# Kernel optimization log

Measured on AMD Instinct MI355X. Metric: run time of the kernel, lower is better.

Reference implementation:

```python
import jax, jax.numpy as jnp
import numpy as np

N_NODES = 100000

def _gcn_norm(edge_index, num_nodes):
    # add self-loops, compute symmetric normalization coeffs per edge
    loops = jnp.arange(num_nodes, dtype=edge_index.dtype)
    src = jnp.concatenate([edge_index[0], loops])
    dst = jnp.concatenate([edge_index[1], loops])
    deg = jax.ops.segment_sum(jnp.ones_like(dst, dtype=jnp.float32), dst,
                              num_segments=num_nodes)
    dinv = jnp.where(deg > 0, jax.lax.rsqrt(deg), 0.0)
    norm = dinv[src] * dinv[dst]  # [E + N]
    return src, dst, norm

def _gcn_conv(x, W, b, src, dst, norm, num_nodes):
    h = x @ W                              # [N, out] transform first (PyG order)
    msg = h[src] * norm[:, None]           # gather + scale
    out = jax.ops.segment_sum(msg, dst, num_segments=num_nodes)  # scatter-add
    return out + b

def setup_inputs() -> dict:
    key = jax.random.key(0)
    k1, k2, k3, k4 = jax.random.split(key, 4)
    F_in, H, C = 128, 64, 40
    x = jax.random.normal(k1, (N_NODES, F_in), dtype=jnp.float32)
    edge_index = jax.random.randint(k2, (2, 1600000), 0, N_NODES, dtype=jnp.int64)
    W1 = jax.random.normal(k3, (F_in, H), dtype=jnp.float32) / np.sqrt(F_in)
    b1 = jnp.zeros((H,), dtype=jnp.float32)
    W2 = jax.random.normal(k4, (H, C), dtype=jnp.float32) / np.sqrt(H)
    b2 = jnp.zeros((C,), dtype=jnp.float32)
    return {"x": x, "edge_index": edge_index, "W1": W1, "b1": b1, "W2": W2, "b2": b2}

def reference(x, edge_index, W1, b1, W2, b2):
    num_nodes = x.shape[0]
    src, dst, norm = _gcn_norm(edge_index, num_nodes)
    h = _gcn_conv(x, W1, b1, src, dst, norm, num_nodes)
    h = jax.nn.relu(h)
    # dropout is identity in eval mode (training=False)
    h = _gcn_conv(h, W2, b2, src, dst, norm, num_nodes)
    return jax.nn.log_softmax(h, axis=1)
```

## Files before the change

### kernel.cpp

```cpp
#include <hip/hip_runtime.h>
#include <math.h>

#define NPB 256
#define BSH 8
#define MAXNB 400
#define BIN_CHUNK 8192
#define HIST_CHUNK 16384

typedef __attribute__((ext_vector_type(8))) short bf16x8;
typedef __attribute__((ext_vector_type(4))) float f32x4;
typedef __attribute__((ext_vector_type(2))) float f32x2;

__device__ __forceinline__ unsigned short f2bf(float f){
  unsigned int u = __float_as_uint(f);
  unsigned int r = (u + 0x7FFFu + ((u >> 16) & 1u)) >> 16;
  return (unsigned short)r;
}

__device__ __forceinline__ bf16x8 cvt8(float4 a, float4 b){
  union { unsigned u[4]; bf16x8 v; } r;
  asm("v_cvt_pk_bf16_f32 %0, %1, %2" : "=v"(r.u[0]) : "v"(a.x), "v"(a.y));
  asm("v_cvt_pk_bf16_f32 %0, %1, %2" : "=v"(r.u[1]) : "v"(a.z), "v"(a.w));
  asm("v_cvt_pk_bf16_f32 %0, %1, %2" : "=v"(r.u[2]) : "v"(b.x), "v"(b.y));
  asm("v_cvt_pk_bf16_f32 %0, %1, %2" : "=v"(r.u[3]) : "v"(b.z), "v"(b.w));
  return r.v;
}

__global__ void k_prep(const float* __restrict__ W1, const float* __restrict__ W2,
                       unsigned short* __restrict__ w1t, unsigned short* __restrict__ w2t,
                       int* __restrict__ bcnt, int NB){
  int t = threadIdx.x;
  if(blockIdx.x == 0){
    for(int i = t; i < 8192; i += 256){
      int k = i >> 6, f = i & 63;
      w1t[f*128 + k] = f2bf(W1[i]);
    }
  } else {
    for(int i = t; i < 3072; i += 256){
      int c = i >> 6, k = i & 63;
      w2t[c*64 + k] = (c < 40) ? f2bf(W2[k*40 + c]) : (unsigned short)0;
    }
    for(int i = t; i < NB; i += 256) bcnt[i] = 0;
  }
}


__global__ __launch_bounds__(256) void k_bhist(const int* __restrict__ dst, int E,
                                               int* __restrict__ bcnt, int NB){
  __shared__ int l[MAXNB];
  int t = threadIdx.x;
  int base = blockIdx.x*HIST_CHUNK;
  int end = base + HIST_CHUNK; if(end > E) end = E;
  for(int b = t; b < NB; b += 256) l[b] = 0;
  __syncthreads();
  for(int i = base + t; i < end; i += 256) atomicAdd(&l[dst[i] >> BSH], 1);
  __syncthreads();
  for(int b = t; b < NB; b += 256){ int c = l[b]; if(c) atomicAdd(&bcnt[b], c); }
}

__global__ void k_bscan(const int* __restrict__ bcnt, int* __restrict__ bofs,
                        int* __restrict__ bcur, int NB, int E){
  __shared__ int sh[1024];
  int t = threadIdx.x;
  int c0 = (2*t   < NB) ? bcnt[2*t]   : 0;
  int c1 = (2*t+1 < NB) ? bcnt[2*t+1] : 0;
  sh[t] = c0 + c1; __syncthreads();
  for(int off = 1; off < 1024; off <<= 1){
    int v = (t >= off) ? sh[t - off] : 0;
    __syncthreads();
    sh[t] += v;
    __syncthreads();
  }
  int pairEx = sh[t] - (c0 + c1);
  if(2*t   < NB){ bofs[2*t]   = pairEx;      bcur[2*t]   = pairEx; }
  if(2*t+1 < NB){ bofs[2*t+1] = pairEx + c0; bcur[2*t+1] = pairEx + c0; }
  if(t == 0) bofs[NB] = E;
}

__global__ __launch_bounds__(256) void k_binpass(const int* __restrict__ src,
                          const int* __restrict__ dst, int E,
                          int* __restrict__ bcur, unsigned int* __restrict__ binned, int NB){
  __shared__ int lcnt[MAXNB];
  __shared__ int lpos[MAXNB];
  int t = threadIdx.x;
  int base = blockIdx.x * BIN_CHUNK;
  int end = base + BIN_CHUNK; if(end > E) end = E;
  for(int b = t; b < NB; b += 256) lcnt[b] = 0;
  __syncthreads();
  for(int i = base + t; i < end; i += 256)
    atomicAdd(&lcnt[dst[i] >> BSH], 1);
  __syncthreads();
  for(int b = t; b < NB; b += 256){
    int c = lcnt[b];
    lpos[b] = c ? atomicAdd(&bcur[b], c) : 0;
  }
  __syncthreads();
  for(int i = base + t; i < end; i += 256){
    int d = dst[i];
    int b = d >> BSH;
    unsigned int rec = (unsigned int)src[i] | ((unsigned int)(d & (NPB-1)) << 17);
    int p = atomicAdd(&lpos[b], 1);
    binned[p] = rec;
  }
}

__global__ __launch_bounds__(256) void k_bscatter(const unsigned int* __restrict__ binned,
     const int* __restrict__ bofs, int* __restrict__ csr, int* __restrict__ row_ofs,
     float* __restrict__ dinv, int N, int E, int NB){
  __shared__ int lcnt[NPB];
  __shared__ int lofs[NPB];
  __shared__ int lcur[NPB];
  __shared__ int wsum[4];
  int b = blockIdx.x, t = threadIdx.x;
  int beg = bofs[b], end = bofs[b+1];
  lcnt[t] = 0;
  __syncthreads();
  for(int i = beg + t; i < end; i += 256) atomicAdd(&lcnt[binned[i] >> 17], 1);
  __syncthreads();
  int c = lcnt[t];
  int lane = t & 63, wid = t >> 6;
  int v = c;
  #pragma unroll
  for(int off = 1; off < 64; off <<= 1){
    int nv = __shfl_up(v, off, 64);
    if(lane >= off) v += nv;
  }
  if(lane == 63) wsum[wid] = v;
  __syncthreads();
  int wpre = 0;
  #pragma unroll
  for(int k2 = 0; k2 < 4; k2++) if(k2 < wid) wpre += wsum[k2];
  int ex = wpre + v - c;
  lofs[t] = beg + ex; lcur[t] = 0;
  int node = (b << BSH) + t;
  if(node < N){
    row_ofs[node] = beg + ex;
    dinv[node] = rsqrtf((float)(c + 1));
  }
  __syncthreads();
  for(int i = beg + t; i < end; i += 256){
    unsigned int rec = binned[i];
    int dl = rec >> 17;
    int pos = lofs[dl] + atomicAdd(&lcur[dl], 1);
    csr[pos] = (int)(rec & 0x1FFFFu);
  }
  if(b == NB-1 && t == 0) row_ofs[N] = E;
}

__global__ __launch_bounds__(256) void k_gemm1(const float* __restrict__ x,
                        const unsigned short* __restrict__ w1t,
                        const float* __restrict__ dinv, unsigned int* __restrict__ g1, int n){
  __shared__ unsigned short xs[128*136];
  __shared__ unsigned short wt[64*136];
  int tid = threadIdx.x;
  int nodeBase = blockIdx.x*128;
  for(int i = tid; i < 1024; i += 256){
    int f = i >> 4, seg = i & 15;
    *(uint4*)&wt[f*136 + seg*8] = *(const uint4*)&w1t[f*128 + seg*8];
  }
  {
    const float4* x4 = (const float4*)x;
    for(int i = tid; i < 2048; i += 256){
      int node = i >> 4, seg = i & 15;
      float4 va = make_float4(0.f,0.f,0.f,0.f), vb = va;
      if(nodeBase + node < n){
        va = x4[(size_t)(nodeBase + node)*32 + seg*2];
        vb = x4[(size_t)(nodeBase + node)*32 + seg*2 + 1];
      }
      *(bf16x8*)&xs[node*136 + seg*8] = cvt8(va, vb);
    }
  }
  __syncthreads();

  int w = tid >> 6, lane = tid & 63;
  int ml = lane & 15, q = lane >> 4;
  int n0 = nodeBase + w*32 + ml;
  int n1 = n0 + 16;
  bool vn0 = n0 < n, vn1 = n1 < n;

  f32x4 a00 = {0.f,0.f,0.f,0.f}, a01 = {0.f,0.f,0.f,0.f},
        a02 = {0.f,0.f,0.f,0.f}, a03 = {0.f,0.f,0.f,0.f};
  f32x4 a10 = {0.f,0.f,0.f,0.f}, a11 = {0.f,0.f,0.f,0.f},
        a12 = {0.f,0.f,0.f,0.f}, a13 = {0.f,0.f,0.f,0.f};
  const unsigned short* brow = &xs[(w*32 + ml)*136 + q*8];
  const unsigned short* arow = &wt[ml*136 + q*8];
  #pragma unroll
  for(int s = 0; s < 4; s++){
    bf16x8 bb0 = *(const bf16x8*)(brow +        s*32);
    bf16x8 bb1 = *(const bf16x8*)(brow + 2176 + s*32);
    bf16x8 a0 = *(const bf16x8*)(arow +    0 + s*32);
    bf16x8 a1 = *(const bf16x8*)(arow + 2176 + s*32);
    bf16x8 a2 = *(const bf16x8*)(arow + 4352 + s*32);
    bf16x8 a3 = *(const bf16x8*)(arow + 6528 + s*32);
    a00 = __builtin_amdgcn_mfma_f32_16x16x32_bf16(a0, bb0, a00, 0, 0, 0);
    a01 = __builtin_amdgcn_mfma_f32_16x16x32_bf16(a1, bb0, a01, 0, 0, 0);
    a02 = __builtin_amdgcn_mfma_f32_16x16x32_bf16(a2, bb0, a02, 0, 0, 0);
    a03 = __builtin_amdgcn_mfma_f32_16x16x32_bf16(a3, bb0, a03, 0, 0, 0);
    a10 = __builtin_amdgcn_mfma_f32_16x16x32_bf16(a0, bb1, a10, 0, 0, 0);
    a11 = __builtin_amdgcn_mfma_f32_16x16x32_bf16(a1, bb1, a11, 0, 0, 0);
    a12 = __builtin_amdgcn_mfma_f32_16x16x32_bf16(a2, bb1, a12, 0, 0, 0);
    a13 = __builtin_amdgcn_mfma_f32_16x16x32_bf16(a3, bb1, a13, 0, 0, 0);
  }
  if(vn0){
    float dv = dinv[n0];
    unsigned base16 = ((unsigned)n0 << 4) + q;
    int p;
    p = __builtin_amdgcn_cvt_pk_fp8_f32(a00[0]*dv, a00[1]*dv, 0, false);
    p = __builtin_amdgcn_cvt_pk_fp8_f32(a00[2]*dv, a00[3]*dv, p, true);
    g1[base16 +  0] = (unsigned)p;
    p = __builtin_amdgcn_cvt_pk_fp8_f32(a01[0]*dv, a01[1]*dv, 0, false);
    p = __builtin_amdgcn_cvt_pk_fp8_f32(a01[2]*dv, a01[3]*dv, p, true);
    g1[base16 +  4] = (unsigned)p;
    p = __builtin_amdgcn_cvt_pk_fp8_f32(a02[0]*dv, a02[1]*dv, 0, false);
    p = __builtin_amdgcn_cvt_pk_fp8_f32(a02[2]*dv, a02[3]*dv, p, true);
    g1[base16 +  8] = (unsigned)p;
    p = __builtin_amdgcn_cvt_pk_fp8_f32(a03[0]*dv, a03[1]*dv, 0, false);
    p = __builtin_amdgcn_cvt_pk_fp8_f32(a03[2]*dv, a03[3]*dv, p, true);
    g1[base16 + 12] = (unsigned)p;
  }
  if(vn1){
    float dv = dinv[n1];
    unsigned base16 = ((unsigned)n1 << 4) + q;
    int p;
    p = __builtin_amdgcn_cvt_pk_fp8_f32(a10[0]*dv, a10[1]*dv, 0, false);
    p = __builtin_amdgcn_cvt_pk_fp8_f32(a10[2]*dv, a10[3]*dv, p, true);
    g1[base16 +  0] = (unsigned)p;
    p = __builtin_amdgcn_cvt_pk_fp8_f32(a11[0]*dv, a11[1]*dv, 0, false);
    p = __builtin_amdgcn_cvt_pk_fp8_f32(a11[2]*dv, a11[3]*dv, p, true);
    g1[base16 +  4] = (unsigned)p;
    p = __builtin_amdgcn_cvt_pk_fp8_f32(a12[0]*dv, a12[1]*dv, 0, false);
    p = __builtin_amdgcn_cvt_pk_fp8_f32(a12[2]*dv, a12[3]*dv, p, true);
    g1[base16 +  8] = (unsigned)p;
    p = __builtin_amdgcn_cvt_pk_fp8_f32(a13[0]*dv, a13[1]*dv, 0, false);
    p = __builtin_amdgcn_cvt_pk_fp8_f32(a13[2]*dv, a13[3]*dv, p, true);
    g1[base16 + 12] = (unsigned)p;
  }
}

__global__ __launch_bounds__(256) void k_agg1g2(const unsigned* __restrict__ g1,
    const int* __restrict__ row_ofs, const int* __restrict__ csr,
    const float* __restrict__ dinv, const float* __restrict__ b1,
    const unsigned short* __restrict__ w2t, unsigned char* __restrict__ g2, int n){
  __shared__ unsigned short us[64*72];
  __shared__ unsigned short ws2[48*72];
  int t = threadIdx.x;
  int nodeBase = blockIdx.x*64;
  for(int i = t; i < 384; i += 256){
    int row = i >> 3, seg = i & 7;
    *(uint4*)&ws2[row*72 + seg*8] = *(const uint4*)&w2t[row*64 + seg*8];
  }
  int lane = t & 63;
  int f = lane & 15;
  int bq = (lane & 48) << 2;
  int qg = t >> 4;
  float4 bb1 = ((const float4*)b1)[f];
  #pragma unroll 1
  for(int i = 0; i < 4; i++){
    int node = nodeBase + qg*4 + i;
    int lrow = qg*4 + i;
    if(node < n){
      int beg = row_ofs[node], end = row_ofs[node+1];
      unsigned v = g1[((unsigned)node << 4) + f];
      f32x2 s01 = __builtin_amdgcn_cvt_pk_f32_fp8(v, false);
      f32x2 s23 = __builtin_amdgcn_cvt_pk_f32_fp8(v, true);
      for(int e = beg; e < end; e += 16){
        int rem = end - e; if(rem > 16) rem = 16;
        int idxv = (f < rem) ? csr[e + f] : 0;
        int j = 0;
        for(; j + 4 <= rem; j += 4){
          int r0 = __builtin_amdgcn_ds_bpermute(bq + ((j+0) << 2), idxv);
          int r1 = __builtin_amdgcn_ds_bpermute(bq + ((j+1) << 2), idxv);
          int r2 = __builtin_amdgcn_ds_bpermute(bq + ((j+2) << 2), idxv);
          int r3 = __builtin_amdgcn_ds_bpermute(bq + ((j+3) << 2), idxv);
          unsigned v0 = g1[((unsigned)r0 << 4) + f];
          unsigned v1 = g1[((unsigned)r1 << 4) + f];
          unsigned v2 = g1[((unsigned)r2 << 4) + f];
          unsigned v3 = g1[((unsigned)r3 << 4) + f];
          s01 += __builtin_amdgcn_cvt_pk_f32_fp8(v0, false);
          s23 += __builtin_amdgcn_cvt_pk_f32_fp8(v0, true);
          s01 += __builtin_amdgcn_cvt_pk_f32_fp8(v1, false);
          s23 += __builtin_amdgcn_cvt_pk_f32_fp8(v1, true);
          s01 += __builtin_amdgcn_cvt_pk_f32_fp8(v2, false);
          s23 += __builtin_amdgcn_cvt_pk_f32_fp8(v2, true);
          s01 += __builtin_amdgcn_cvt_pk_f32_fp8(v3, false);
          s23 += __builtin_amdgcn_cvt_pk_f32_fp8(v3, true);
        }
        for(; j < rem; j++){
          int r0 = __builtin_amdgcn_ds_bpermute(bq + (j << 2), idxv);
          unsigned v0 = g1[((unsigned)r0 << 4) + f];
          s01 += __builtin_amdgcn_cvt_pk_f32_fp8(v0, false);
          s23 += __builtin_amdgcn_cvt_pk_f32_fp8(v0, true);
        }
      }
      float dv = dinv[node];
      float h0 = fmaxf(fmaf(dv, s01.x, bb1.x), 0.f);
      float h1 = fmaxf(fmaf(dv, s01.y, bb1.y), 0.f);
      float h2 = fmaxf(fmaf(dv, s23.x, bb1.z), 0.f);
      float h3 = fmaxf(fmaf(dv, s23.y, bb1.w), 0.f);
      unsigned p0, p1;
      asm("v_cvt_pk_bf16_f32 %0, %1, %2" : "=v"(p0) : "v"(dv*h0), "v"(dv*h1));
      asm("v_cvt_pk_bf16_f32 %0, %1, %2" : "=v"(p1) : "v"(dv*h2), "v"(dv*h3));
      *(uint2*)&us[lrow*72 + f*4] = make_uint2(p0, p1);
    } else {
      *(uint2*)&us[lrow*72 + f*4] = make_uint2(0u, 0u);
    }
  }
  __syncthreads();
  int w = t >> 6;
  int ml = lane & 15, q = lane >> 4;
  f32x4 acc0 = {0.f,0.f,0.f,0.f}, acc1 = {0.f,0.f,0.f,0.f}, acc2 = {0.f,0.f,0.f,0.f};
  const unsigned short* brow = &us[(w*16 + ml)*72 + q*8];
  const unsigned short* a0r = &ws2[ml*72 + q*8];
  #pragma unroll
  for(int s = 0; s < 2; s++){
    bf16x8 bb = *(const bf16x8*)(brow + s*32);
    bf16x8 a0 = *(const bf16x8*)(a0r +    0 + s*32);
    bf16x8 a1 = *(const bf16x8*)(a0r + 1152 + s*32);
    bf16x8 a2 = *(const bf16x8*)(a0r + 2304 + s*32);
    acc0 = __builtin_amdgcn_mfma_f32_16x16x32_bf16(a0, bb, acc0, 0, 0, 0);
    acc1 = __builtin_amdgcn_mfma_f32_16x16x32_bf16(a1, bb, acc1, 0, 0, 0);
    acc2 = __builtin_amdgcn_mfma_f32_16x16x32_bf16(a2, bb, acc2, 0, 0, 0);
  }
  int node = nodeBase + w*16 + ml;
  if(node < n){
    unsigned* gd = (unsigned*)g2;
    unsigned rb = (unsigned)node*10u + q;
    int p;
    p = __builtin_amdgcn_cvt_pk_fp8_f32(acc0[0], acc0[1], 0, false);
    p = __builtin_amdgcn_cvt_pk_fp8_f32(acc0[2], acc0[3], p, true);
    gd[rb + 0] = (unsigned)p;
    p = __builtin_amdgcn_cvt_pk_fp8_f32(acc1[0], acc1[1], 0, false);
    p = __builtin_amdgcn_cvt_pk_fp8_f32(acc1[2], acc1[3], p, true);
    gd[rb + 4] = (unsigned)p;
    if(q < 2){
      p = __builtin_amdgcn_cvt_pk_fp8_f32(acc2[0], acc2[1], 0, false);
      p = __builtin_amdgcn_cvt_pk_fp8_f32(acc2[2], acc2[3], p, true);
      gd[rb + 8] = (unsigned)p;
    }
  }
}

__global__ __launch_bounds__(256) void k_agg2(const unsigned char* __restrict__ g2,
     const int* __restrict__ row_ofs, const int* __restrict__ csr,
     const float* __restrict__ dinv, const float* __restrict__ b2,
     float* __restrict__ out, int N){
  int t = threadIdx.x;
  int lane = t & 63;
  int f = lane & 15;
  int fc = (f < 10) ? f : 0;
  int bq = (lane & 48) << 2;
  int node = blockIdx.x*16 + (t >> 4);
  if(node >= N) return;
  int beg = row_ofs[node], end = row_ofs[node+1];
  const unsigned* gd = (const unsigned*)g2;
  unsigned v = gd[(unsigned)node*10u + fc];
  f32x2 s01 = __builtin_amdgcn_cvt_pk_f32_fp8(v, false);
  f32x2 s23 = __builtin_amdgcn_cvt_pk_f32_fp8(v, true);
  for(int e = beg; e < end; e += 16){
    int rem = end - e; if(rem > 16) rem = 16;
    int idxv = (f < rem) ? csr[e + f] : 0;
    int j = 0;
    for(; j + 4 <= rem; j += 4){
      int r0 = __builtin_amdgcn_ds_bpermute(bq + ((j+0) << 2), idxv);
      int r1 = __builtin_amdgcn_ds_bpermute(bq + ((j+1) << 2), idxv);
      int r2 = __builtin_amdgcn_ds_bpermute(bq + ((j+2) << 2), idxv);
      int r3 = __builtin_amdgcn_ds_bpermute(bq + ((j+3) << 2), idxv);
      unsigned v0 = gd[(unsigned)r0*10u + fc];
      unsigned v1 = gd[(unsigned)r1*10u + fc];
      unsigned v2 = gd[(unsigned)r2*10u + fc];
      unsigned v3 = gd[(unsigned)r3*10u + fc];
      s01 += __builtin_amdgcn_cvt_pk_f32_fp8(v0, false);
      s23 += __builtin_amdgcn_cvt_pk_f32_fp8(v0, true);
      s01 += __builtin_amdgcn_cvt_pk_f32_fp8(v1, false);
      s23 += __builtin_amdgcn_cvt_pk_f32_fp8(v1, true);
      s01 += __builtin_amdgcn_cvt_pk_f32_fp8(v2, false);
      s23 += __builtin_amdgcn_cvt_pk_f32_fp8(v2, true);
      s01 += __builtin_amdgcn_cvt_pk_f32_fp8(v3, false);
      s23 += __builtin_amdgcn_cvt_pk_f32_fp8(v3, true);
    }
    for(; j < rem; j++){
      int r0 = __builtin_amdgcn_ds_bpermute(bq + (j << 2), idxv);
      unsigned v0 = gd[(unsigned)r0*10u + fc];
      s01 += __builtin_amdgcn_cvt_pk_f32_fp8(v0, false);
      s23 += __builtin_amdgcn_cvt_pk_f32_fp8(v0, true);
    }
  }
  float dv = dinv[node];
  float4 bb = ((const float4*)b2)[fc];
  float l0 = fmaf(dv, s01.x, bb.x);
  float l1 = fmaf(dv, s01.y, bb.y);
  float l2 = fmaf(dv, s23.x, bb.z);
  float l3 = fmaf(dv, s23.y, bb.w);
  bool valid = (f < 10);
  float m = valid ? fmaxf(fmaxf(l0,l1), fmaxf(l2,l3)) : -INFINITY;
  m = fmaxf(m, __shfl_xor(m,1,64)); m = fmaxf(m, __shfl_xor(m,2,64));
  m = fmaxf(m, __shfl_xor(m,4,64)); m = fmaxf(m, __shfl_xor(m,8,64));
  float ex = valid ? (expf(l0-m)+expf(l1-m)) + (expf(l2-m)+expf(l3-m)) : 0.f;
  ex += __shfl_xor(ex,1,64); ex += __shfl_xor(ex,2,64);
  ex += __shfl_xor(ex,4,64); ex += __shfl_xor(ex,8,64);
  float ll = logf(ex);
  if(valid){
    ((float4*)out)[(unsigned)node*10u + f] = make_float4(l0-m-ll, l1-m-ll, l2-m-ll, l3-m-ll);
  }
}


extern "C" void kernel_launch(void* const* d_in, const int* in_sizes, int n_in,
                              void* d_out, int out_size, void* d_ws, size_t ws_size,
                              hipStream_t stream){
  const float* x  = (const float*)d_in[0];
  const int*   ei = (const int*)  d_in[1];
  const float* W1 = (const float*)d_in[2];
  const float* b1 = (const float*)d_in[3];
  const float* W2 = (const float*)d_in[4];
  const float* b2 = (const float*)d_in[5];
  float* out = (float*)d_out;

  int N = in_sizes[0] / 128;
  int E = in_sizes[1] / 2;
  const int* src = ei;
  const int* dst = ei + E;
  int NB = (N + NPB - 1) >> BSH;

  char* w = (char*)d_ws;
  auto alloc = [&](size_t bytes) -> char* {
    char* p = w;
    w += (bytes + 511) & ~(size_t)511;
    return p;
  };
  int*   bcnt    = (int*)  alloc((size_t)NB*4);
  int*   bofs    = (int*)  alloc((size_t)(NB+1)*4);
  int*   bcur    = (int*)  alloc((size_t)NB*4);
  int*   row_ofs = (int*)  alloc((size_t)(N+1)*4);
  float* dinv    = (float*)alloc((size_t)N*4);
  unsigned int* binned = (unsigned int*)alloc((size_t)E*4);
  int*   csr     = (int*)  alloc((size_t)E*4);
  unsigned int*   g1 = (unsigned int*)  alloc((size_t)N*64);
  unsigned char*  g2 = (unsigned char*) alloc((size_t)N*40);
  unsigned short* w1t = (unsigned short*)alloc((size_t)64*128*2);
  unsigned short* w2t = (unsigned short*)alloc((size_t)48*64*2);

  k_prep    <<<2, 256, 0, stream>>>(W1, W2, w1t, w2t, bcnt, NB);
  k_bhist   <<<(E+HIST_CHUNK-1)/HIST_CHUNK, 256, 0, stream>>>(dst, E, bcnt, NB);
  k_bscan   <<<1, 1024, 0, stream>>>(bcnt, bofs, bcur, NB, E);
  k_binpass <<<(E+BIN_CHUNK-1)/BIN_CHUNK, 256, 0, stream>>>(src, dst, E, bcur, binned, NB);
  k_bscatter<<<NB, 256, 0, stream>>>(binned, bofs, csr, row_ofs, dinv, N, E, NB);

  k_gemm1   <<<(N+127)/128, 256, 0, stream>>>(x, w1t, dinv, g1, N);
  k_agg1g2  <<<(N+63)/64, 256, 0, stream>>>(g1, row_ofs, csr, dinv, b1, w2t, g2, N);
  k_agg2    <<<(N+15)/16, 256, 0, stream>>>(g2, row_ofs, csr, dinv, b2, out, N);
}
```

Before: 228.1 us.

## Add dynamic per-block node work queues to aggregation kernels and fold prep into histogram

Both aggregation kernels now hand out nodes dynamically. Each 16-lane quarter-wave claims the next node from a shared atomic counter and processes one 16-edge chunk per iteration, so uneven node degrees balance within the block. agg2 now covers 64 nodes per block instead of 16. The weight prep kernel is merged into the histogram launch as extra blocks, and bcnt zeroing moves to a memset. Histogram and bin chunk sizes are halved or quartered to create more blocks. The change adds an atomic, a shuffle and wave-wide vote overhead to every loop iteration.

```diff
diff --git a/kernel.cpp b/kernel.cpp
--- a/kernel.cpp
+++ b/kernel.cpp
@@ -4,8 +4,8 @@
 #define NPB 256
 #define BSH 8
 #define MAXNB 400
-#define BIN_CHUNK 8192
-#define HIST_CHUNK 16384
+#define BIN_CHUNK 4096
+#define HIST_CHUNK 4096
 
 typedef __attribute__((ext_vector_type(8))) short bf16x8;
 typedef __attribute__((ext_vector_type(4))) float f32x4;
@@ -26,36 +26,36 @@
   return r.v;
 }
 
-__global__ void k_prep(const float* __restrict__ W1, const float* __restrict__ W2,
-                       unsigned short* __restrict__ w1t, unsigned short* __restrict__ w2t,
-                       int* __restrict__ bcnt, int NB){
-  int t = threadIdx.x;
-  if(blockIdx.x == 0){
-    for(int i = t; i < 8192; i += 256){
-      int k = i >> 6, f = i & 63;
-      w1t[f*128 + k] = f2bf(W1[i]);
-    }
-  } else {
-    for(int i = t; i < 3072; i += 256){
-      int c = i >> 6, k = i & 63;
-      w2t[c*64 + k] = (c < 40) ? f2bf(W2[k*40 + c]) : (unsigned short)0;
-    }
-    for(int i = t; i < NB; i += 256) bcnt[i] = 0;
-  }
-}
-
 
 __global__ __launch_bounds__(256) void k_bhist(const int* __restrict__ dst, int E,
-                                               int* __restrict__ bcnt, int NB){
+                                               int* __restrict__ bcnt, int NB, int NBH,
+                                               const float* __restrict__ W1,
+                                               const float* __restrict__ W2,
+                                               unsigned short* __restrict__ w1t,
+                                               unsigned short* __restrict__ w2t){
   __shared__ int l[MAXNB];
-  int t = threadIdx.x;
-  int base = blockIdx.x*HIST_CHUNK;
+  int t = threadIdx.x, b = blockIdx.x;
+  if(b >= NBH){
+    if(b == NBH){
+      for(int i = t; i < 8192; i += 256){
+        int k = i >> 6, f = i & 63;
+        w1t[f*128 + k] = f2bf(W1[i]);
+      }
+    } else {
+      for(int i = t; i < 3072; i += 256){
+        int c = i >> 6, k = i & 63;
+        w2t[c*64 + k] = (c < 40) ? f2bf(W2[k*40 + c]) : (unsigned short)0;
+      }
+    }
+    return;
+  }
+  int base = b*HIST_CHUNK;
   int end = base + HIST_CHUNK; if(end > E) end = E;
-  for(int b = t; b < NB; b += 256) l[b] = 0;
+  for(int i = t; i < NB; i += 256) l[i] = 0;
   __syncthreads();
   for(int i = base + t; i < end; i += 256) atomicAdd(&l[dst[i] >> BSH], 1);
   __syncthreads();
-  for(int b = t; b < NB; b += 256){ int c = l[b]; if(c) atomicAdd(&bcnt[b], c); }
+  for(int i = t; i < NB; i += 256){ int c = l[i]; if(c) atomicAdd(&bcnt[i], c); }
 }
 
 __global__ void k_bscan(const int* __restrict__ bcnt, int* __restrict__ bofs,
@@ -243,39 +243,60 @@
     const unsigned short* __restrict__ w2t, unsigned char* __restrict__ g2, int n){
   __shared__ unsigned short us[64*72];
   __shared__ unsigned short ws2[48*72];
+  __shared__ int nctr;
   int t = threadIdx.x;
   int nodeBase = blockIdx.x*64;
   for(int i = t; i < 384; i += 256){
     int row = i >> 3, seg = i & 7;
     *(uint4*)&ws2[row*72 + seg*8] = *(const uint4*)&w2t[row*64 + seg*8];
   }
+  if(t == 0) nctr = 0;
+  __syncthreads();
   int lane = t & 63;
-  int f = lane & 15;
-  int bq = (lane & 48) << 2;
-  int qg = t >> 4;
-  float4 bb1 = ((const float4*)b1)[f];
-  #pragma unroll 1
-  for(int i = 0; i < 4; i++){
-    int node = nodeBase + qg*4 + i;
-    int lrow = qg*4 + i;
-    if(node < n){
-      int beg = row_ofs[node], end = row_ofs[node+1];
-      unsigned v = g1[((unsigned)node << 4) + f];
-      f32x2 s01 = __builtin_amdgcn_cvt_pk_f32_fp8(v, false);
-      f32x2 s23 = __builtin_amdgcn_cvt_pk_f32_fp8(v, true);
-      for(int e = beg; e < end; e += 16){
-        int rem = end - e; if(rem > 16) rem = 16;
-        int idxv = (f < rem) ? csr[e + f] : 0;
+  int lq = lane & 15;
+  int qsrc = lane & 48;
+  int bq = qsrc << 2;
+  float4 bb1 = ((const float4*)b1)[lq];
+  int myi = -1;
+  int e = 0, eend = 0;
+  float dv = 0.f;
+  f32x2 s01 = {0.f,0.f}, s23 = {0.f,0.f};
+  for(;;){
+    if(myi == -1){
+      int tk = 0;
+      if(lq == 0) tk = atomicAdd(&nctr, 1);
+      tk = __shfl(tk, qsrc, 64);
+      if(tk >= 64){ myi = -2; }
+      else {
+        myi = tk;
+        int node = nodeBase + tk;
+        if(node < n){
+          e = row_ofs[node]; eend = row_ofs[node+1];
+          dv = dinv[node];
+          unsigned v = g1[((unsigned)node << 4) + lq];
+          s01 = __builtin_amdgcn_cvt_pk_f32_fp8(v, false);
+          s23 = __builtin_amdgcn_cvt_pk_f32_fp8(v, true);
+        } else {
+          e = 0; eend = 0; dv = 0.f;
+          s01 = (f32x2){0.f,0.f}; s23 = (f32x2){0.f,0.f};
+        }
+      }
+    }
+    if(__all(myi == -2)) break;
+    if(myi >= 0){
+      int rem = eend - e; if(rem > 16) rem = 16;
+      if(rem > 0){
+        int idxv = (lq < rem) ? csr[e + lq] : 0;
         int j = 0;
         for(; j + 4 <= rem; j += 4){
           int r0 = __builtin_amdgcn_ds_bpermute(bq + ((j+0) << 2), idxv);
           int r1 = __builtin_amdgcn_ds_bpermute(bq + ((j+1) << 2), idxv);
           int r2 = __builtin_amdgcn_ds_bpermute(bq + ((j+2) << 2), idxv);
           int r3 = __builtin_amdgcn_ds_bpermute(bq + ((j+3) << 2), idxv);
-          unsigned v0 = g1[((unsigned)r0 << 4) + f];
-          unsigned v1 = g1[((unsigned)r1 << 4) + f];
-          unsigned v2 = g1[((unsigned)r2 << 4) + f];
-          unsigned v3 = g1[((unsigned)r3 << 4) + f];
+          unsigned v0 = g1[((unsigned)r0 << 4) + lq];
+          unsigned v1 = g1[((unsigned)r1 << 4) + lq];
+          unsigned v2 = g1[((unsigned)r2 << 4) + lq];
+          unsigned v3 = g1[((unsigned)r3 << 4) + lq];
           s01 += __builtin_amdgcn_cvt_pk_f32_fp8(v0, false);
           s23 += __builtin_amdgcn_cvt_pk_f32_fp8(v0, true);
           s01 += __builtin_amdgcn_cvt_pk_f32_fp8(v1, false);
@@ -287,22 +308,23 @@
         }
         for(; j < rem; j++){
           int r0 = __builtin_amdgcn_ds_bpermute(bq + (j << 2), idxv);
-          unsigned v0 = g1[((unsigned)r0 << 4) + f];
+          unsigned v0 = g1[((unsigned)r0 << 4) + lq];
           s01 += __builtin_amdgcn_cvt_pk_f32_fp8(v0, false);
           s23 += __builtin_amdgcn_cvt_pk_f32_fp8(v0, true);
         }
-      }
-      float dv = dinv[node];
-      float h0 = fmaxf(fmaf(dv, s01.x, bb1.x), 0.f);
-      float h1 = fmaxf(fmaf(dv, s01.y, bb1.y), 0.f);
-      float h2 = fmaxf(fmaf(dv, s23.x, bb1.z), 0.f);
-      float h3 = fmaxf(fmaf(dv, s23.y, bb1.w), 0.f);
-      unsigned p0, p1;
-      asm("v_cvt_pk_bf16_f32 %0, %1, %2" : "=v"(p0) : "v"(dv*h0), "v"(dv*h1));
-      asm("v_cvt_pk_bf16_f32 %0, %1, %2" : "=v"(p1) : "v"(dv*h2), "v"(dv*h3));
-      *(uint2*)&us[lrow*72 + f*4] = make_uint2(p0, p1);
-    } else {
-      *(uint2*)&us[lrow*72 + f*4] = make_uint2(0u, 0u);
+        e += rem;
+      }
+      if(e >= eend){
+        float h0 = fmaxf(fmaf(dv, s01.x, bb1.x), 0.f);
+        float h1 = fmaxf(fmaf(dv, s01.y, bb1.y), 0.f);
+        float h2 = fmaxf(fmaf(dv, s23.x, bb1.z), 0.f);
+        float h3 = fmaxf(fmaf(dv, s23.y, bb1.w), 0.f);
+        unsigned p0, p1;
+        asm("v_cvt_pk_bf16_f32 %0, %1, %2" : "=v"(p0) : "v"(dv*h0), "v"(dv*h1));
+        asm("v_cvt_pk_bf16_f32 %0, %1, %2" : "=v"(p1) : "v"(dv*h2), "v"(dv*h3));
+        *(uint2*)&us[myi*72 + lq*4] = make_uint2(p0, p1);
+        myi = -1;
+      }
     }
   }
   __syncthreads();
@@ -344,63 +366,97 @@
      const int* __restrict__ row_ofs, const int* __restrict__ csr,
      const float* __restrict__ dinv, const float* __restrict__ b2,
      float* __restrict__ out, int N){
+  __shared__ int nctr;
   int t = threadIdx.x;
+  if(t == 0) nctr = 0;
+  __syncthreads();
   int lane = t & 63;
-  int f = lane & 15;
-  int fc = (f < 10) ? f : 0;
-  int bq = (lane & 48) << 2;
-  int node = blockIdx.x*16 + (t >> 4);
-  if(node >= N) return;
-  int beg = row_ofs[node], end = row_ofs[node+1];
+  int lq = lane & 15;
+  int fc = (lq < 10) ? lq : 0;
+  int qsrc = lane & 48;
+  int bq = qsrc << 2;
+  int nodeBase = blockIdx.x*64;
   const unsigned* gd = (const unsigned*)g2;
-  unsigned v = gd[(unsigned)node*10u + fc];
-  f32x2 s01 = __builtin_amdgcn_cvt_pk_f32_fp8(v, false);
-  f32x2 s23 = __builtin_amdgcn_cvt_pk_f32_fp8(v, true);
-  for(int e = beg; e < end; e += 16){
-    int rem = end - e; if(rem > 16) rem = 16;
-    int idxv = (f < rem) ? csr[e + f] : 0;
-    int j = 0;
-    for(; j + 4 <= rem; j += 4){
-      int r0 = __builtin_amdgcn_ds_bpermute(bq + ((j+0) << 2), idxv);
-      int r1 = __builtin_amdgcn_ds_bpermute(bq + ((j+1) << 2), idxv);
-      int r2 = __builtin_amdgcn_ds_bpermute(bq + ((j+2) << 2), idxv);
-      int r3 = __builtin_amdgcn_ds_bpermute(bq + ((j+3) << 2), idxv);
-      unsigned v0 = gd[(unsigned)r0*10u + fc];
-      unsigned v1 = gd[(unsigned)r1*10u + fc];
-      unsigned v2 = gd[(unsigned)r2*10u + fc];
-      unsigned v3 = gd[(unsigned)r3*10u + fc];
-      s01 += __builtin_amdgcn_cvt_pk_f32_fp8(v0, false);
-      s23 += __builtin_amdgcn_cvt_pk_f32_fp8(v0, true);
-      s01 += __builtin_amdgcn_cvt_pk_f32_fp8(v1, false);
-      s23 += __builtin_amdgcn_cvt_pk_f32_fp8(v1, true);
-      s01 += __builtin_amdgcn_cvt_pk_f32_fp8(v2, false);
-      s23 += __builtin_amdgcn_cvt_pk_f32_fp8(v2, true);
-      s01 += __builtin_amdgcn_cvt_pk_f32_fp8(v3, false);
-      s23 += __builtin_amdgcn_cvt_pk_f32_fp8(v3, true);
-    }
-    for(; j < rem; j++){
-      int r0 = __builtin_amdgcn_ds_bpermute(bq + (j << 2), idxv);
-      unsigned v0 = gd[(unsigned)r0*10u + fc];
-      s01 += __builtin_amdgcn_cvt_pk_f32_fp8(v0, false);
-      s23 += __builtin_amdgcn_cvt_pk_f32_fp8(v0, true);
-    }
-  }
-  float dv = dinv[node];
-  float4 bb = ((const float4*)b2)[fc];
-  float l0 = fmaf(dv, s01.x, bb.x);
-  float l1 = fmaf(dv, s01.y, bb.y);
-  float l2 = fmaf(dv, s23.x, bb.z);
-  float l3 = fmaf(dv, s23.y, bb.w);
-  bool valid = (f < 10);
-  float m = valid ? fmaxf(fmaxf(l0,l1), fmaxf(l2,l3)) : -INFINITY;
-  m = fmaxf(m, __shfl_xor(m,1,64)); m = fmaxf(m, __shfl_xor(m,2,64));
-  m = fmaxf(m, __shfl_xor(m,4,64)); m = fmaxf(m, __shfl_xor(m,8,64));
-  float ex = valid ? (expf(l0-m)+expf(l1-m)) + (expf(l2-m)+expf(l3-m)) : 0.f;
-  ex += __shfl_xor(ex,1,64); ex += __shfl_xor(ex,2,64);
-  ex += __shfl_xor(ex,4,64); ex += __shfl_xor(ex,8,64);
-  float ll = logf(ex);
-  if(valid){
-    ((float4*)out)[(unsigned)node*10u + f] = make_float4(l0-m-ll, l1-m-ll, l2-m-ll, l3-m-ll);
+  float4 bb2 = ((const float4*)b2)[fc];
+  int myi = -1;
+  int e = 0, eend = 0;
+  float dv = 0.f;
+  f32x2 s01 = {0.f,0.f}, s23 = {0.f,0.f};
+  for(;;){
+    if(myi == -1){
+      int tk = 0;
+      if(lq == 0) tk = atomicAdd(&nctr, 1);
+      tk = __shfl(tk, qsrc, 64);
+      if(tk >= 64){ myi = -2; }
+      else {
+        myi = tk;
+        int node = nodeBase + tk;
+        if(node < N){
+          e = row_ofs[node]; eend = row_ofs[node+1];
+          dv = dinv[node];
+          unsigned v = gd[(unsigned)node*10u + fc];
+          s01 = __builtin_amdgcn_cvt_pk_f32_fp8(v, false);
+          s23 = __builtin_amdgcn_cvt_pk_f32_fp8(v, true);
+        } else {
+          e = 0; eend = 0; dv = 0.f;
+          s01 = (f32x2){0.f,0.f}; s23 = (f32x2){0.f,0.f};
+        }
+      }
+    }
+    if(__all(myi == -2)) break;
+    if(myi >= 0){
+      int rem = eend - e; if(rem > 16) rem = 16;
+      if(rem > 0){
+        int idxv = (lq < rem) ? csr[e + lq] : 0;
+        int j = 0;
+        for(; j + 4 <= rem; j += 4){
+          int r0 = __builtin_amdgcn_ds_bpermute(bq + ((j+0) << 2), idxv);
+          int r1 = __builtin_amdgcn_ds_bpermute(bq + ((j+1) << 2), idxv);
+          int r2 = __builtin_amdgcn_ds_bpermute(bq + ((j+2) << 2), idxv);
+          int r3 = __builtin_amdgcn_ds_bpermute(bq + ((j+3) << 2), idxv);
+          unsigned v0 = gd[(unsigned)r0*10u + fc];
+          unsigned v1 = gd[(unsigned)r1*10u + fc];
+          unsigned v2 = gd[(unsigned)r2*10u + fc];
+          unsigned v3 = gd[(unsigned)r3*10u + fc];
+          s01 += __builtin_amdgcn_cvt_pk_f32_fp8(v0, false);
+          s23 += __builtin_amdgcn_cvt_pk_f32_fp8(v0, true);
+          s01 += __builtin_amdgcn_cvt_pk_f32_fp8(v1, false);
+          s23 += __builtin_amdgcn_cvt_pk_f32_fp8(v1, true);
+          s01 += __builtin_amdgcn_cvt_pk_f32_fp8(v2, false);
+          s23 += __builtin_amdgcn_cvt_pk_f32_fp8(v2, true);
+          s01 += __builtin_amdgcn_cvt_pk_f32_fp8(v3, false);
+          s23 += __builtin_amdgcn_cvt_pk_f32_fp8(v3, true);
+        }
+        for(; j < rem; j++){
+          int r0 = __builtin_amdgcn_ds_bpermute(bq + (j << 2), idxv);
+          unsigned v0 = gd[(unsigned)r0*10u + fc];
+          s01 += __builtin_amdgcn_cvt_pk_f32_fp8(v0, false);
+          s23 += __builtin_amdgcn_cvt_pk_f32_fp8(v0, true);
+        }
+        e += rem;
+      }
+      if(e >= eend){
+        int node = nodeBase + myi;
+        if(node < N){
+          float l0 = fmaf(dv, s01.x, bb2.x);
+          float l1 = fmaf(dv, s01.y, bb2.y);
+          float l2 = fmaf(dv, s23.x, bb2.z);
+          float l3 = fmaf(dv, s23.y, bb2.w);
+          bool valid = (lq < 10);
+          float m = valid ? fmaxf(fmaxf(l0,l1), fmaxf(l2,l3)) : -INFINITY;
+          m = fmaxf(m, __shfl_xor(m,1,64)); m = fmaxf(m, __shfl_xor(m,2,64));
+          m = fmaxf(m, __shfl_xor(m,4,64)); m = fmaxf(m, __shfl_xor(m,8,64));
+          float ex = valid ? (expf(l0-m)+expf(l1-m)) + (expf(l2-m)+expf(l3-m)) : 0.f;
+          ex += __shfl_xor(ex,1,64); ex += __shfl_xor(ex,2,64);
+          ex += __shfl_xor(ex,4,64); ex += __shfl_xor(ex,8,64);
+          float ll = logf(ex);
+          if(valid){
+            ((float4*)out)[(unsigned)node*10u + lq] = make_float4(l0-m-ll, l1-m-ll, l2-m-ll, l3-m-ll);
+          }
+        }
+        myi = -1;
+      }
+    }
   }
 }
 
@@ -440,13 +496,15 @@
   unsigned short* w1t = (unsigned short*)alloc((size_t)64*128*2);
   unsigned short* w2t = (unsigned short*)alloc((size_t)48*64*2);
 
-  k_prep    <<<2, 256, 0, stream>>>(W1, W2, w1t, w2t, bcnt, NB);
-  k_bhist   <<<(E+HIST_CHUNK-1)/HIST_CHUNK, 256, 0, stream>>>(dst, E, bcnt, NB);
+  int NBH = (E + HIST_CHUNK - 1)/HIST_CHUNK;
+
+  hipMemsetAsync(bcnt, 0, (size_t)NB*4, stream);
+  k_bhist   <<<NBH+2, 256, 0, stream>>>(dst, E, bcnt, NB, NBH, W1, W2, w1t, w2t);
   k_bscan   <<<1, 1024, 0, stream>>>(bcnt, bofs, bcur, NB, E);
   k_binpass <<<(E+BIN_CHUNK-1)/BIN_CHUNK, 256, 0, stream>>>(src, dst, E, bcur, binned, NB);
   k_bscatter<<<NB, 256, 0, stream>>>(binned, bofs, csr, row_ofs, dinv, N, E, NB);
 
   k_gemm1   <<<(N+127)/128, 256, 0, stream>>>(x, w1t, dinv, g1, N);
   k_agg1g2  <<<(N+63)/64, 256, 0, stream>>>(g1, row_ofs, csr, dinv, b1, w2t, g2, N);
-  k_agg2    <<<(N+15)/16, 256, 0, stream>>>(g2, row_ofs, csr, dinv, b2, out, N);
-}
+  k_agg2    <<<(N+63)/64, 256, 0, stream>>>(g2, row_ofs, csr, dinv, b2, out, N);
+}
```

Result: no change. 229.4 us (+0.6%).

## Fold weight prep into histogram kernel, shrink chunk sizes, unroll full gathers

Applied to the files above, without the earlier changes.

Merges the weight transpose/convert kernel into the histogram launch as two extra blocks and zeroes the bucket counts with a memset instead of a separate kernel. It halves the bin chunk size and quarters the histogram chunk size to launch more blocks. It also adds a fully unrolled 16-neighbour gather path in both aggregation kernels so more loads are in flight at once. The intent is less launch overhead and more memory-level parallelism, at the cost of higher register pressure and more global atomics from the extra blocks.

```diff
diff --git a/kernel.cpp b/kernel.cpp
--- a/kernel.cpp
+++ b/kernel.cpp
@@ -4,8 +4,8 @@
 #define NPB 256
 #define BSH 8
 #define MAXNB 400
-#define BIN_CHUNK 8192
-#define HIST_CHUNK 16384
+#define BIN_CHUNK 4096
+#define HIST_CHUNK 4096
 
 typedef __attribute__((ext_vector_type(8))) short bf16x8;
 typedef __attribute__((ext_vector_type(4))) float f32x4;
@@ -26,36 +26,36 @@
   return r.v;
 }
 
-__global__ void k_prep(const float* __restrict__ W1, const float* __restrict__ W2,
-                       unsigned short* __restrict__ w1t, unsigned short* __restrict__ w2t,
-                       int* __restrict__ bcnt, int NB){
-  int t = threadIdx.x;
-  if(blockIdx.x == 0){
-    for(int i = t; i < 8192; i += 256){
-      int k = i >> 6, f = i & 63;
-      w1t[f*128 + k] = f2bf(W1[i]);
+
+__global__ __launch_bounds__(256) void k_bhist(const int* __restrict__ dst, int E,
+                                               int* __restrict__ bcnt, int NB, int NBH,
+                                               const float* __restrict__ W1,
+                                               const float* __restrict__ W2,
+                                               unsigned short* __restrict__ w1t,
+                                               unsigned short* __restrict__ w2t){
+  __shared__ int l[MAXNB];
+  int t = threadIdx.x, b = blockIdx.x;
+  if(b >= NBH){
+    if(b == NBH){
+      for(int i = t; i < 8192; i += 256){
+        int k = i >> 6, f = i & 63;
+        w1t[f*128 + k] = f2bf(W1[i]);
+      }
+    } else {
+      for(int i = t; i < 3072; i += 256){
+        int c = i >> 6, k = i & 63;
+        w2t[c*64 + k] = (c < 40) ? f2bf(W2[k*40 + c]) : (unsigned short)0;
+      }
     }
-  } else {
-    for(int i = t; i < 3072; i += 256){
-      int c = i >> 6, k = i & 63;
-      w2t[c*64 + k] = (c < 40) ? f2bf(W2[k*40 + c]) : (unsigned short)0;
-    }
-    for(int i = t; i < NB; i += 256) bcnt[i] = 0;
-  }
-}
-
-
-__global__ __launch_bounds__(256) void k_bhist(const int* __restrict__ dst, int E,
-                                               int* __restrict__ bcnt, int NB){
-  __shared__ int l[MAXNB];
-  int t = threadIdx.x;
-  int base = blockIdx.x*HIST_CHUNK;
+    return;
+  }
+  int base = b*HIST_CHUNK;
   int end = base + HIST_CHUNK; if(end > E) end = E;
-  for(int b = t; b < NB; b += 256) l[b] = 0;
+  for(int i = t; i < NB; i += 256) l[i] = 0;
   __syncthreads();
   for(int i = base + t; i < end; i += 256) atomicAdd(&l[dst[i] >> BSH], 1);
   __syncthreads();
-  for(int b = t; b < NB; b += 256){ int c = l[b]; if(c) atomicAdd(&bcnt[b], c); }
+  for(int i = t; i < NB; i += 256){ int c = l[i]; if(c) atomicAdd(&bcnt[i], c); }
 }
 
 __global__ void k_bscan(const int* __restrict__ bcnt, int* __restrict__ bofs,
@@ -266,30 +266,82 @@
       for(int e = beg; e < end; e += 16){
         int rem = end - e; if(rem > 16) rem = 16;
         int idxv = (f < rem) ? csr[e + f] : 0;
-        int j = 0;
-        for(; j + 4 <= rem; j += 4){
-          int r0 = __builtin_amdgcn_ds_bpermute(bq + ((j+0) << 2), idxv);
-          int r1 = __builtin_amdgcn_ds_bpermute(bq + ((j+1) << 2), idxv);
-          int r2 = __builtin_amdgcn_ds_bpermute(bq + ((j+2) << 2), idxv);
-          int r3 = __builtin_amdgcn_ds_bpermute(bq + ((j+3) << 2), idxv);
-          unsigned v0 = g1[((unsigned)r0 << 4) + f];
-          unsigned v1 = g1[((unsigned)r1 << 4) + f];
-          unsigned v2 = g1[((unsigned)r2 << 4) + f];
-          unsigned v3 = g1[((unsigned)r3 << 4) + f];
-          s01 += __builtin_amdgcn_cvt_pk_f32_fp8(v0, false);
-          s23 += __builtin_amdgcn_cvt_pk_f32_fp8(v0, true);
-          s01 += __builtin_amdgcn_cvt_pk_f32_fp8(v1, false);
-          s23 += __builtin_amdgcn_cvt_pk_f32_fp8(v1, true);
-          s01 += __builtin_amdgcn_cvt_pk_f32_fp8(v2, false);
-          s23 += __builtin_amdgcn_cvt_pk_f32_fp8(v2, true);
-          s01 += __builtin_amdgcn_cvt_pk_f32_fp8(v3, false);
-          s23 += __builtin_amdgcn_cvt_pk_f32_fp8(v3, true);
-        }
-        for(; j < rem; j++){
-          int r0 = __builtin_amdgcn_ds_bpermute(bq + (j << 2), idxv);
-          unsigned v0 = g1[((unsigned)r0 << 4) + f];
-          s01 += __builtin_amdgcn_cvt_pk_f32_fp8(v0, false);
-          s23 += __builtin_amdgcn_cvt_pk_f32_fp8(v0, true);
+        if(rem == 16){
+          int r0,r1,r2,r3,r4,r5,r6,r7,r8,r9,r10,r11,r12,r13,r14,r15;
+          r0  = __builtin_amdgcn_ds_bpermute(bq +  0, idxv);
+          r1  = __builtin_amdgcn_ds_bpermute(bq +  4, idxv);
+          r2  = __builtin_amdgcn_ds_bpermute(bq +  8, idxv);
+          r3  = __builtin_amdgcn_ds_bpermute(bq + 12, idxv);
+          r4  = __builtin_amdgcn_ds_bpermute(bq + 16, idxv);
+          r5  = __builtin_amdgcn_ds_bpermute(bq + 20, idxv);
+          r6  = __builtin_amdgcn_ds_bpermute(bq + 24, idxv);
+          r7  = __builtin_amdgcn_ds_bpermute(bq + 28, idxv);
+          r8  = __builtin_amdgcn_ds_bpermute(bq + 32, idxv);
+          r9  = __builtin_amdgcn_ds_bpermute(bq + 36, idxv);
+          r10 = __builtin_amdgcn_ds_bpermute(bq + 40, idxv);
+          r11 = __builtin_amdgcn_ds_bpermute(bq + 44, idxv);
+          r12 = __builtin_amdgcn_ds_bpermute(bq + 48, idxv);
+          r13 = __builtin_amdgcn_ds_bpermute(bq + 52, idxv);
+          r14 = __builtin_amdgcn_ds_bpermute(bq + 56, idxv);
+          r15 = __builtin_amdgcn_ds_bpermute(bq + 60, idxv);
+          unsigned w0  = g1[((unsigned)r0  << 4) + f];
+          unsigned w1  = g1[((unsigned)r1  << 4) + f];
+          unsigned w2  = g1[((unsigned)r2  << 4) + f];
+          unsigned w3  = g1[((unsigned)r3  << 4) + f];
+          unsigned w4  = g1[((unsigned)r4  << 4) + f];
+          unsigned w5  = g1[((unsigned)r5  << 4) + f];
+          unsigned w6  = g1[((unsigned)r6  << 4) + f];
+          unsigned w7  = g1[((unsigned)r7  << 4) + f];
+          unsigned w8  = g1[((unsigned)r8  << 4) + f];
+          unsigned w9  = g1[((unsigned)r9  << 4) + f];
+          unsigned w10 = g1[((unsigned)r10 << 4) + f];
+          unsigned w11 = g1[((unsigned)r11 << 4) + f];
+          unsigned w12 = g1[((unsigned)r12 << 4) + f];
+          unsigned w13 = g1[((unsigned)r13 << 4) + f];
+          unsigned w14 = g1[((unsigned)r14 << 4) + f];
+          unsigned w15 = g1[((unsigned)r15 << 4) + f];
+          s01 += __builtin_amdgcn_cvt_pk_f32_fp8(w0 , false); s23 += __builtin_amdgcn_cvt_pk_f32_fp8(w0 , true);
+          s01 += __builtin_amdgcn_cvt_pk_f32_fp8(w1 , false); s23 += __builtin_amdgcn_cvt_pk_f32_fp8(w1 , true);
+          s01 += __builtin_amdgcn_cvt_pk_f32_fp8(w2 , false); s23 += __builtin_amdgcn_cvt_pk_f32_fp8(w2 , true);
+          s01 += __builtin_amdgcn_cvt_pk_f32_fp8(w3 , false); s23 += __builtin_amdgcn_cvt_pk_f32_fp8(w3 , true);
+          s01 += __builtin_amdgcn_cvt_pk_f32_fp8(w4 , false); s23 += __builtin_amdgcn_cvt_pk_f32_fp8(w4 , true);
+          s01 += __builtin_amdgcn_cvt_pk_f32_fp8(w5 , false); s23 += __builtin_amdgcn_cvt_pk_f32_fp8(w5 , true);
+          s01 += __builtin_amdgcn_cvt_pk_f32_fp8(w6 , false); s23 += __builtin_amdgcn_cvt_pk_f32_fp8(w6 , true);
+          s01 += __builtin_amdgcn_cvt_pk_f32_fp8(w7 , false); s23 += __builtin_amdgcn_cvt_pk_f32_fp8(w7 , true);
+          s01 += __builtin_amdgcn_cvt_pk_f32_fp8(w8 , false); s23 += __builtin_amdgcn_cvt_pk_f32_fp8(w8 , true);
+          s01 += __builtin_amdgcn_cvt_pk_f32_fp8(w9 , false); s23 += __builtin_amdgcn_cvt_pk_f32_fp8(w9 , true);
+          s01 += __builtin_amdgcn_cvt_pk_f32_fp8(w10, false); s23 += __builtin_amdgcn_cvt_pk_f32_fp8(w10, true);
+          s01 += __builtin_amdgcn_cvt_pk_f32_fp8(w11, false); s23 += __builtin_amdgcn_cvt_pk_f32_fp8(w11, true);
+          s01 += __builtin_amdgcn_cvt_pk_f32_fp8(w12, false); s23 += __builtin_amdgcn_cvt_pk_f32_fp8(w12, true);
+          s01 += __builtin_amdgcn_cvt_pk_f32_fp8(w13, false); s23 += __builtin_amdgcn_cvt_pk_f32_fp8(w13, true);
+          s01 += __builtin_amdgcn_cvt_pk_f32_fp8(w14, false); s23 += __builtin_amdgcn_cvt_pk_f32_fp8(w14, true);
+          s01 += __builtin_amdgcn_cvt_pk_f32_fp8(w15, false); s23 += __builtin_amdgcn_cvt_pk_f32_fp8(w15, true);
+        } else {
+          int j = 0;
+          for(; j + 4 <= rem; j += 4){
+            int r0 = __builtin_amdgcn_ds_bpermute(bq + ((j+0) << 2), idxv);
+            int r1 = __builtin_amdgcn_ds_bpermute(bq + ((j+1) << 2), idxv);
+            int r2 = __builtin_amdgcn_ds_bpermute(bq + ((j+2) << 2), idxv);
+            int r3 = __builtin_amdgcn_ds_bpermute(bq + ((j+3) << 2), idxv);
+            unsigned v0 = g1[((unsigned)r0 << 4) + f];
+            unsigned v1 = g1[((unsigned)r1 << 4) + f];
+            unsigned v2 = g1[((unsigned)r2 << 4) + f];
+            unsigned v3 = g1[((unsigned)r3 << 4) + f];
+            s01 += __builtin_amdgcn_cvt_pk_f32_fp8(v0, false);
+            s23 += __builtin_amdgcn_cvt_pk_f32_fp8(v0, true);
+            s01 += __builtin_amdgcn_cvt_pk_f32_fp8(v1, false);
+            s23 += __builtin_amdgcn_cvt_pk_f32_fp8(v1, true);
+            s01 += __builtin_amdgcn_cvt_pk_f32_fp8(v2, false);
+            s23 += __builtin_amdgcn_cvt_pk_f32_fp8(v2, true);
+            s01 += __builtin_amdgcn_cvt_pk_f32_fp8(v3, false);
+            s23 += __builtin_amdgcn_cvt_pk_f32_fp8(v3, true);
+          }
+          for(; j < rem; j++){
+            int r0 = __builtin_amdgcn_ds_bpermute(bq + (j << 2), idxv);
+            unsigned v0 = g1[((unsigned)r0 << 4) + f];
+            s01 += __builtin_amdgcn_cvt_pk_f32_fp8(v0, false);
+            s23 += __builtin_amdgcn_cvt_pk_f32_fp8(v0, true);
+          }
         }
       }
       float dv = dinv[node];
@@ -359,30 +411,82 @@
   for(int e = beg; e < end; e += 16){
     int rem = end - e; if(rem > 16) rem = 16;
     int idxv = (f < rem) ? csr[e + f] : 0;
-    int j = 0;
-    for(; j + 4 <= rem; j += 4){
-      int r0 = __builtin_amdgcn_ds_bpermute(bq + ((j+0) << 2), idxv);
-      int r1 = __builtin_amdgcn_ds_bpermute(bq + ((j+1) << 2), idxv);
-      int r2 = __builtin_amdgcn_ds_bpermute(bq + ((j+2) << 2), idxv);
-      int r3 = __builtin_amdgcn_ds_bpermute(bq + ((j+3) << 2), idxv);
-      unsigned v0 = gd[(unsigned)r0*10u + fc];
-      unsigned v1 = gd[(unsigned)r1*10u + fc];
-      unsigned v2 = gd[(unsigned)r2*10u + fc];
-      unsigned v3 = gd[(unsigned)r3*10u + fc];
-      s01 += __builtin_amdgcn_cvt_pk_f32_fp8(v0, false);
-      s23 += __builtin_amdgcn_cvt_pk_f32_fp8(v0, true);
-      s01 += __builtin_amdgcn_cvt_pk_f32_fp8(v1, false);
-      s23 += __builtin_amdgcn_cvt_pk_f32_fp8(v1, true);
-      s01 += __builtin_amdgcn_cvt_pk_f32_fp8(v2, false);
-      s23 += __builtin_amdgcn_cvt_pk_f32_fp8(v2, true);
-      s01 += __builtin_amdgcn_cvt_pk_f32_fp8(v3, false);
-      s23 += __builtin_amdgcn_cvt_pk_f32_fp8(v3, true);
-    }
-    for(; j < rem; j++){
-      int r0 = __builtin_amdgcn_ds_bpermute(bq + (j << 2), idxv);
-      unsigned v0 = gd[(unsigned)r0*10u + fc];
-      s01 += __builtin_amdgcn_cvt_pk_f32_fp8(v0, false);
-      s23 += __builtin_amdgcn_cvt_pk_f32_fp8(v0, true);
+    if(rem == 16){
+      int r0,r1,r2,r3,r4,r5,r6,r7,r8,r9,r10,r11,r12,r13,r14,r15;
+      r0  = __builtin_amdgcn_ds_bpermute(bq +  0, idxv);
+      r1  = __builtin_amdgcn_ds_bpermute(bq +  4, idxv);
+      r2  = __builtin_amdgcn_ds_bpermute(bq +  8, idxv);
+      r3  = __builtin_amdgcn_ds_bpermute(bq + 12, idxv);
+      r4  = __builtin_amdgcn_ds_bpermute(bq + 16, idxv);
+      r5  = __builtin_amdgcn_ds_bpermute(bq + 20, idxv);
+      r6  = __builtin_amdgcn_ds_bpermute(bq + 24, idxv);
+      r7  = __builtin_amdgcn_ds_bpermute(bq + 28, idxv);
+      r8  = __builtin_amdgcn_ds_bpermute(bq + 32, idxv);
+      r9  = __builtin_amdgcn_ds_bpermute(bq + 36, idxv);
+      r10 = __builtin_amdgcn_ds_bpermute(bq + 40, idxv);
+      r11 = __builtin_amdgcn_ds_bpermute(bq + 44, idxv);
+      r12 = __builtin_amdgcn_ds_bpermute(bq + 48, idxv);
+      r13 = __builtin_amdgcn_ds_bpermute(bq + 52, idxv);
+      r14 = __builtin_amdgcn_ds_bpermute(bq + 56, idxv);
+      r15 = __builtin_amdgcn_ds_bpermute(bq + 60, idxv);
+      unsigned w0  = gd[(unsigned)r0 *10u + fc];
+      unsigned w1  = gd[(unsigned)r1 *10u + fc];
+      unsigned w2  = gd[(unsigned)r2 *10u + fc];
+      unsigned w3  = gd[(unsigned)r3 *10u + fc];
+      unsigned w4  = gd[(unsigned)r4 *10u + fc];
+      unsigned w5  = gd[(unsigned)r5 *10u + fc];
+      unsigned w6  = gd[(unsigned)r6 *10u + fc];
+      unsigned w7  = gd[(unsigned)r7 *10u + fc];
+      unsigned w8  = gd[(unsigned)r8 *10u + fc];
+      unsigned w9  = gd[(unsigned)r9 *10u + fc];
+      unsigned w10 = gd[(unsigned)r10*10u + fc];
+      unsigned w11 = gd[(unsigned)r11*10u + fc];
+      unsigned w12 = gd[(unsigned)r12*10u + fc];
+      unsigned w13 = gd[(unsigned)r13*10u + fc];
+      unsigned w14 = gd[(unsigned)r14*10u + fc];
+      unsigned w15 = gd[(unsigned)r15*10u + fc];
+      s01 += __builtin_amdgcn_cvt_pk_f32_fp8(w0 , false); s23 += __builtin_amdgcn_cvt_pk_f32_fp8(w0 , true);
+      s01 += __builtin_amdgcn_cvt_pk_f32_fp8(w1 , false); s23 += __builtin_amdgcn_cvt_pk_f32_fp8(w1 , true);
+      s01 += __builtin_amdgcn_cvt_pk_f32_fp8(w2 , false); s23 += __builtin_amdgcn_cvt_pk_f32_fp8(w2 , true);
+      s01 += __builtin_amdgcn_cvt_pk_f32_fp8(w3 , false); s23 += __builtin_amdgcn_cvt_pk_f32_fp8(w3 , true);
+      s01 += __builtin_amdgcn_cvt_pk_f32_fp8(w4 , false); s23 += __builtin_amdgcn_cvt_pk_f32_fp8(w4 , true);
+      s01 += __builtin_amdgcn_cvt_pk_f32_fp8(w5 , false); s23 += __builtin_amdgcn_cvt_pk_f32_fp8(w5 , true);
+      s01 += __builtin_amdgcn_cvt_pk_f32_fp8(w6 , false); s23 += __builtin_amdgcn_cvt_pk_f32_fp8(w6 , true);
+      s01 += __builtin_amdgcn_cvt_pk_f32_fp8(w7 , false); s23 += __builtin_amdgcn_cvt_pk_f32_fp8(w7 , true);
+      s01 += __builtin_amdgcn_cvt_pk_f32_fp8(w8 , false); s23 += __builtin_amdgcn_cvt_pk_f32_fp8(w8 , true);
+      s01 += __builtin_amdgcn_cvt_pk_f32_fp8(w9 , false); s23 += __builtin_amdgcn_cvt_pk_f32_fp8(w9 , true);
+      s01 += __builtin_amdgcn_cvt_pk_f32_fp8(w10, false); s23 += __builtin_amdgcn_cvt_pk_f32_fp8(w10, true);
+      s01 += __builtin_amdgcn_cvt_pk_f32_fp8(w11, false); s23 += __builtin_amdgcn_cvt_pk_f32_fp8(w11, true);
+      s01 += __builtin_amdgcn_cvt_pk_f32_fp8(w12, false); s23 += __builtin_amdgcn_cvt_pk_f32_fp8(w12, true);
+      s01 += __builtin_amdgcn_cvt_pk_f32_fp8(w13, false); s23 += __builtin_amdgcn_cvt_pk_f32_fp8(w13, true);
+      s01 += __builtin_amdgcn_cvt_pk_f32_fp8(w14, false); s23 += __builtin_amdgcn_cvt_pk_f32_fp8(w14, true);
+      s01 += __builtin_amdgcn_cvt_pk_f32_fp8(w15, false); s23 += __builtin_amdgcn_cvt_pk_f32_fp8(w15, true);
+    } else {
+      int j = 0;
+      for(; j + 4 <= rem; j += 4){
+        int r0 = __builtin_amdgcn_ds_bpermute(bq + ((j+0) << 2), idxv);
+        int r1 = __builtin_amdgcn_ds_bpermute(bq + ((j+1) << 2), idxv);
+        int r2 = __builtin_amdgcn_ds_bpermute(bq + ((j+2) << 2), idxv);
+        int r3 = __builtin_amdgcn_ds_bpermute(bq + ((j+3) << 2), idxv);
+        unsigned v0 = gd[(unsigned)r0*10u + fc];
+        unsigned v1 = gd[(unsigned)r1*10u + fc];
+        unsigned v2 = gd[(unsigned)r2*10u + fc];
+        unsigned v3 = gd[(unsigned)r3*10u + fc];
+        s01 += __builtin_amdgcn_cvt_pk_f32_fp8(v0, false);
+        s23 += __builtin_amdgcn_cvt_pk_f32_fp8(v0, true);
+        s01 += __builtin_amdgcn_cvt_pk_f32_fp8(v1, false);
+        s23 += __builtin_amdgcn_cvt_pk_f32_fp8(v1, true);
+        s01 += __builtin_amdgcn_cvt_pk_f32_fp8(v2, false);
+        s23 += __builtin_amdgcn_cvt_pk_f32_fp8(v2, true);
+        s01 += __builtin_amdgcn_cvt_pk_f32_fp8(v3, false);
+        s23 += __builtin_amdgcn_cvt_pk_f32_fp8(v3, true);
+      }
+      for(; j < rem; j++){
+        int r0 = __builtin_amdgcn_ds_bpermute(bq + (j << 2), idxv);
+        unsigned v0 = gd[(unsigned)r0*10u + fc];
+        s01 += __builtin_amdgcn_cvt_pk_f32_fp8(v0, false);
+        s23 += __builtin_amdgcn_cvt_pk_f32_fp8(v0, true);
+      }
     }
   }
   float dv = dinv[node];
@@ -440,8 +544,10 @@
   unsigned short* w1t = (unsigned short*)alloc((size_t)64*128*2);
   unsigned short* w2t = (unsigned short*)alloc((size_t)48*64*2);
 
-  k_prep    <<<2, 256, 0, stream>>>(W1, W2, w1t, w2t, bcnt, NB);
-  k_bhist   <<<(E+HIST_CHUNK-1)/HIST_CHUNK, 256, 0, stream>>>(dst, E, bcnt, NB);
+  int NBH = (E + HIST_CHUNK - 1)/HIST_CHUNK;
+
+  hipMemsetAsync(bcnt, 0, (size_t)NB*4, stream);
+  k_bhist   <<<NBH+2, 256, 0, stream>>>(dst, E, bcnt, NB, NBH, W1, W2, w1t, w2t);
   k_bscan   <<<1, 1024, 0, stream>>>(bcnt, bofs, bcur, NB, E);
   k_binpass <<<(E+BIN_CHUNK-1)/BIN_CHUNK, 256, 0, stream>>>(src, dst, E, bcur, binned, NB);
   k_bscatter<<<NB, 256, 0, stream>>>(binned, bofs, csr, row_ofs, dinv, N, E, NB);
```

Measured after the change: 219.1 us. 4.0% less time.
